# Optimization experiments

Measured on AMD Instinct MI355X. Metric: run time of the kernel, lower is better.

The kernel has to match this reference:

```python
import jax, jax.numpy as jnp
import numpy as np


def setup_inputs() -> dict:
    key = jax.random.key(0)
    k1, k2, k3, k4 = jax.random.split(key, 4)
    B, T, C, H = 32, 2048, 384, 64
    x = jax.random.normal(k1, (B, T, C), dtype=jnp.float32)
    # nn.Linear(C, H, bias=False): weight stored [H, C], applied as x @ W.T.
    # We store the transposed [C, H] form directly.
    s = 1.0 / np.sqrt(C)
    Wk = jax.random.normal(k2, (C, H), dtype=jnp.float32) * s
    Wq = jax.random.normal(k3, (C, H), dtype=jnp.float32) * s
    Wv = jax.random.normal(k4, (C, H), dtype=jnp.float32) * s
    return {"x": x, "Wk": Wk, "Wq": Wq, "Wv": Wv}


def reference(x, Wk, Wq, Wv):
    # x: [B, T, C]; Wk/Wq/Wv: [C, H]
    T = x.shape[1]
    H = Wk.shape[1]
    k = jnp.einsum('btc,ch->bth', x, Wk)
    q = jnp.einsum('btc,ch->bth', x, Wq)
    v = jnp.einsum('btc,ch->bth', x, Wv)
    scale = H ** (-0.5)
    scores = jnp.einsum('bth,bsh->bts', q, k) * scale  # [B, T, T]
    causal = jnp.tril(jnp.ones((T, T), dtype=bool))
    scores = jnp.where(causal, scores, -jnp.inf)
    attn = jax.nn.softmax(scores, axis=-1)
    # dropout is identity in eval mode
    out = jnp.einsum('bts,bsh->bth', attn, v)  # [B, T, H]
    return out
```

## Files before the change

kernel.cpp:

```cpp
#include <hip/hip_runtime.h>

typedef __bf16 bf16_8 __attribute__((ext_vector_type(8)));
typedef __bf16 bf16_4 __attribute__((ext_vector_type(4)));
typedef float  f32x4  __attribute__((ext_vector_type(4)));

#define NB 32
#define NT 2048
#define NC 384
#define NH 64

static __device__ __forceinline__ f32x4 mfma16(bf16_8 a, bf16_8 b, f32x4 c) {
  return __builtin_amdgcn_mfma_f32_16x16x32_bf16(a, b, c, 0, 0, 0);
}

__global__ void pack_w_kernel(const float* __restrict__ Wk, const float* __restrict__ Wq,
                              const float* __restrict__ Wv, __bf16* __restrict__ Wt) {
  int idx = blockIdx.x * 256 + threadIdx.x;
  if (idx >= 192 * NC) return;
  int n = idx / NC, k = idx % NC;
  int sel = n >> 6, h = n & 63;
  const float* W = (sel == 0) ? Wq : (sel == 1 ? Wk : Wv);
  float v = W[k * NH + h];
  if (sel == 0) v *= 0.125f;
  Wt[idx] = (__bf16)v;
}

__launch_bounds__(256)
__global__ void qkv_kernel(const float* __restrict__ x, const __bf16* __restrict__ Wt,
                           __bf16* __restrict__ Q, __bf16* __restrict__ K,
                           __bf16* __restrict__ Vt) {
  __shared__ __bf16 Vl[64][136];

  const int tid  = threadIdx.x;
  const int lane = tid & 63, wq = tid >> 6;
  const int quad = lane >> 4, l16 = lane & 15;
  const int rowblk = blockIdx.x * 128;
  const int rbase  = rowblk + wq * 32;

  f32x4 acc[2][12];
  #pragma unroll
  for (int m = 0; m < 2; ++m)
    #pragma unroll
    for (int n = 0; n < 12; ++n) acc[m][n] = f32x4{0.f, 0.f, 0.f, 0.f};

  for (int kc = 0; kc < 12; ++kc) {
    const int k0 = kc * 32 + quad * 8;
    bf16_8 a[2];
    #pragma unroll
    for (int m = 0; m < 2; ++m) {
      const float* xp = x + (size_t)(rbase + m * 16 + l16) * NC + k0;
      f32x4 x0 = *(const f32x4*)xp;
      f32x4 x1 = *(const f32x4*)(xp + 4);
      bf16_8 t;
      t[0] = (__bf16)x0[0]; t[1] = (__bf16)x0[1]; t[2] = (__bf16)x0[2]; t[3] = (__bf16)x0[3];
      t[4] = (__bf16)x1[0]; t[5] = (__bf16)x1[1]; t[6] = (__bf16)x1[2]; t[7] = (__bf16)x1[3];
      a[m] = t;
    }
    #pragma unroll
    for (int n = 0; n < 12; ++n) {
      bf16_8 b = *(const bf16_8*)(Wt + (size_t)(n * 16 + l16) * NC + k0);
      acc[0][n] = mfma16(a[0], b, acc[0][n]);
      acc[1][n] = mfma16(a[1], b, acc[1][n]);
    }
  }

  #pragma unroll
  for (int m = 0; m < 2; ++m)
    #pragma unroll
    for (int n = 0; n < 8; ++n)
      #pragma unroll
      for (int r = 0; r < 4; ++r) {
        int row = rbase + m * 16 + quad * 4 + r;
        int h = (n & 3) * 16 + l16;
        __bf16 bv = (__bf16)acc[m][n][r];
        if (n < 4) Q[(size_t)row * NH + h] = bv;
        else       K[(size_t)row * NH + h] = bv;
      }

  #pragma unroll
  for (int m = 0; m < 2; ++m)
    #pragma unroll
    for (int n = 8; n < 12; ++n) {
      int h = (n - 8) * 16 + l16;
      int t0 = wq * 32 + m * 16 + quad * 4;
      bf16_4 p;
      p[0] = (__bf16)acc[m][n][0]; p[1] = (__bf16)acc[m][n][1];
      p[2] = (__bf16)acc[m][n][2]; p[3] = (__bf16)acc[m][n][3];
      *(bf16_4*)&Vl[h][t0] = p;
    }
  __syncthreads();
  {
    int h = tid >> 2, seg = tid & 3;
    int bb = rowblk >> 11, t0 = (rowblk & (NT - 1)) + seg * 32;
    const __bf16* src = &Vl[h][seg * 32];
    __bf16* dst = Vt + ((size_t)(bb * NH + h)) * NT + t0;
    #pragma unroll
    for (int i = 0; i < 4; ++i) ((uint4*)dst)[i] = ((const uint4*)src)[i];
  }
}

__launch_bounds__(256)
__global__ void attn_kernel(const __bf16* __restrict__ Q, const __bf16* __restrict__ K,
                            const __bf16* __restrict__ Vt, float* __restrict__ out) {
  __shared__ __bf16 Ks[64][72];
  __shared__ __bf16 Vs[64][72];
  __shared__ __bf16 Ps[4][16][72];

  const int tid  = threadIdx.x;
  const int lane = tid & 63, wq = tid >> 6;
  const int quad = lane >> 4, l16 = lane & 15;
  const int b  = blockIdx.x >> 5;
  const int qt = 31 - (blockIdx.x & 31);
  const int q0 = qt * 64;

  const float NEG_INF = -__builtin_inff();

  const __bf16* qrow = Q + ((size_t)(b * NT + q0 + wq * 16 + l16)) * NH + quad * 8;
  bf16_8 qf0 = *(const bf16_8*)qrow;
  bf16_8 qf1 = *(const bf16_8*)(qrow + 32);

  f32x4 o[4];
  #pragma unroll
  for (int i = 0; i < 4; ++i) o[i] = f32x4{0.f, 0.f, 0.f, 0.f};
  float m_i = NEG_INF, l_i = 0.f;

  const int r = tid >> 2, seg = tid & 3;
  const __bf16* Kg = K  + (size_t)b * NT * NH;
  const __bf16* Vg = Vt + (size_t)b * NH * NT;

  for (int s0 = 0; s0 <= q0; s0 += 64) {
    __syncthreads();
    {
      const uint4* sK = (const uint4*)(Kg + (size_t)(s0 + r) * NH + seg * 16);
      uint4 k0v = sK[0], k1v = sK[1];
      *(uint4*)&Ks[r][seg * 16]     = k0v;
      *(uint4*)&Ks[r][seg * 16 + 8] = k1v;
      const uint4* sV = (const uint4*)(Vg + (size_t)r * NT + s0 + seg * 16);
      uint4 v0v = sV[0], v1v = sV[1];
      *(uint4*)&Vs[r][seg * 16]     = v0v;
      *(uint4*)&Vs[r][seg * 16 + 8] = v1v;
    }
    __syncthreads();

    f32x4 s[4];
    #pragma unroll
    for (int st = 0; st < 4; ++st) {
      bf16_8 a0 = *(const bf16_8*)&Ks[st * 16 + l16][quad * 8];
      bf16_8 a1 = *(const bf16_8*)&Ks[st * 16 + l16][quad * 8 + 32];
      f32x4 accv = f32x4{0.f, 0.f, 0.f, 0.f};
      accv = mfma16(a0, qf0, accv);
      accv = mfma16(a1, qf1, accv);
      s[st] = accv;
    }

    if (s0 == q0) {
      int qg = wq * 16 + l16;
      #pragma unroll
      for (int st = 0; st < 4; ++st)
        #pragma unroll
        for (int rr = 0; rr < 4; ++rr) {
          int sg = st * 16 + quad * 4 + rr;
          if (sg > qg) s[st][rr] = NEG_INF;
        }
    }

    float mx = NEG_INF;
    #pragma unroll
    for (int st = 0; st < 4; ++st)
      #pragma unroll
      for (int rr = 0; rr < 4; ++rr) mx = fmaxf(mx, s[st][rr]);
    mx = fmaxf(mx, __shfl_xor(mx, 16));
    mx = fmaxf(mx, __shfl_xor(mx, 32));
    float m_new = fmaxf(m_i, mx);
    float alpha = __expf(m_i - m_new);

    float lsum = 0.f;
    #pragma unroll
    for (int st = 0; st < 4; ++st) {
      bf16_4 pk;
      #pragma unroll
      for (int rr = 0; rr < 4; ++rr) {
        float p = __expf(s[st][rr] - m_new);
        lsum += p;
        pk[rr] = (__bf16)p;
      }
      *(bf16_4*)&Ps[wq][l16][st * 16 + quad * 4] = pk;
    }
    lsum += __shfl_xor(lsum, 16);
    lsum += __shfl_xor(lsum, 32);
    l_i = l_i * alpha + lsum;
    m_i = m_new;

    f32x4 av;
    #pragma unroll
    for (int rr = 0; rr < 4; ++rr) av[rr] = __shfl(alpha, quad * 4 + rr);
    #pragma unroll
    for (int nt = 0; nt < 4; ++nt)
      #pragma unroll
      for (int rr = 0; rr < 4; ++rr) o[nt][rr] *= av[rr];

    bf16_8 pa0 = *(const bf16_8*)&Ps[wq][l16][quad * 8];
    bf16_8 pa1 = *(const bf16_8*)&Ps[wq][l16][quad * 8 + 32];
    #pragma unroll
    for (int nt = 0; nt < 4; ++nt) {
      bf16_8 b0 = *(const bf16_8*)&Vs[nt * 16 + l16][quad * 8];
      bf16_8 b1 = *(const bf16_8*)&Vs[nt * 16 + l16][quad * 8 + 32];
      o[nt] = mfma16(pa0, b0, o[nt]);
      o[nt] = mfma16(pa1, b1, o[nt]);
    }
  }

  f32x4 lv;
  #pragma unroll
  for (int rr = 0; rr < 4; ++rr) lv[rr] = 1.f / __shfl(l_i, quad * 4 + rr);
  float* op = out + ((size_t)(b * NT + q0 + wq * 16 + quad * 4)) * NH + l16;
  #pragma unroll
  for (int nt = 0; nt < 4; ++nt)
    #pragma unroll
    for (int rr = 0; rr < 4; ++rr)
      op[(size_t)rr * NH + nt * 16] = o[nt][rr] * lv[rr];
}

extern "C" void kernel_launch(void* const* d_in, const int* in_sizes, int n_in,
                              void* d_out, int out_size, void* d_ws, size_t ws_size,
                              hipStream_t stream) {
  const float* x  = (const float*)d_in[0];
  const float* Wk = (const float*)d_in[1];
  const float* Wq = (const float*)d_in[2];
  const float* Wv = (const float*)d_in[3];
  float* out = (float*)d_out;

  char* ws = (char*)d_ws;
  __bf16* Wt  = (__bf16*)ws;
  __bf16* Qb  = (__bf16*)(ws + 256 * 1024);
  __bf16* Kb  = Qb + (size_t)NB * NT * NH;
  __bf16* Vtb = Kb + (size_t)NB * NT * NH;

  pack_w_kernel<<<288, 256, 0, stream>>>(Wk, Wq, Wv, Wt);
  qkv_kernel<<<512, 256, 0, stream>>>(x, Wt, Qb, Kb, Vtb);
  attn_kernel<<<NB * 32, 256, 0, stream>>>(Qb, Kb, Vtb, out);
}
```

Before: 256.8 us.

## Double-buffer K/V tiles, pair causal query tiles per block, shrink QKV tiles

The attention kernel now double-buffers K/V tiles in shared memory. Global loads for the next tile are issued before the current tile's compute and written to the other buffer afterwards, which removes one barrier per iteration. Each block now handles a long and a short causal query tile (qt and 31-qt) to balance work across 512 blocks. The QKV projection uses 64-row blocks with register prefetch of x and a 4-wave occupancy hint, doubling the grid. The cost is more LDS per attention block and fewer attention blocks.

Result: faster. 251.3 us (-2.2%).

```diff
diff --git a/kernel.cpp b/kernel.cpp
--- a/kernel.cpp
+++ b/kernel.cpp
@@ -25,200 +25,219 @@
   Wt[idx] = (__bf16)v;
 }
 
-__launch_bounds__(256)
+__launch_bounds__(256, 4)
 __global__ void qkv_kernel(const float* __restrict__ x, const __bf16* __restrict__ Wt,
                            __bf16* __restrict__ Q, __bf16* __restrict__ K,
                            __bf16* __restrict__ Vt) {
-  __shared__ __bf16 Vl[64][136];
+  __shared__ __bf16 Vl[64][72];
 
   const int tid  = threadIdx.x;
   const int lane = tid & 63, wq = tid >> 6;
   const int quad = lane >> 4, l16 = lane & 15;
-  const int rowblk = blockIdx.x * 128;
-  const int rbase  = rowblk + wq * 32;
-
-  f32x4 acc[2][12];
+  const int rowblk = blockIdx.x * 64;
+  const int rbase  = rowblk + wq * 16;
+
+  f32x4 acc[12];
   #pragma unroll
-  for (int m = 0; m < 2; ++m)
-    #pragma unroll
-    for (int n = 0; n < 12; ++n) acc[m][n] = f32x4{0.f, 0.f, 0.f, 0.f};
+  for (int n = 0; n < 12; ++n) acc[n] = f32x4{0.f, 0.f, 0.f, 0.f};
+
+  const float* xrow = x + (size_t)(rbase + l16) * NC;
+  f32x4 x0 = *(const f32x4*)(xrow + quad * 8);
+  f32x4 x1 = *(const f32x4*)(xrow + quad * 8 + 4);
 
   for (int kc = 0; kc < 12; ++kc) {
-    const int k0 = kc * 32 + quad * 8;
-    bf16_8 a[2];
-    #pragma unroll
-    for (int m = 0; m < 2; ++m) {
-      const float* xp = x + (size_t)(rbase + m * 16 + l16) * NC + k0;
-      f32x4 x0 = *(const f32x4*)xp;
-      f32x4 x1 = *(const f32x4*)(xp + 4);
-      bf16_8 t;
-      t[0] = (__bf16)x0[0]; t[1] = (__bf16)x0[1]; t[2] = (__bf16)x0[2]; t[3] = (__bf16)x0[3];
-      t[4] = (__bf16)x1[0]; t[5] = (__bf16)x1[1]; t[6] = (__bf16)x1[2]; t[7] = (__bf16)x1[3];
-      a[m] = t;
-    }
+    f32x4 nx0, nx1;
+    if (kc < 11) {
+      const float* xp = xrow + (kc + 1) * 32 + quad * 8;
+      nx0 = *(const f32x4*)xp;
+      nx1 = *(const f32x4*)(xp + 4);
+    }
+    bf16_8 a;
+    a[0] = (__bf16)x0[0]; a[1] = (__bf16)x0[1]; a[2] = (__bf16)x0[2]; a[3] = (__bf16)x0[3];
+    a[4] = (__bf16)x1[0]; a[5] = (__bf16)x1[1]; a[6] = (__bf16)x1[2]; a[7] = (__bf16)x1[3];
+    const __bf16* wp = Wt + (size_t)l16 * NC + kc * 32 + quad * 8;
     #pragma unroll
     for (int n = 0; n < 12; ++n) {
-      bf16_8 b = *(const bf16_8*)(Wt + (size_t)(n * 16 + l16) * NC + k0);
-      acc[0][n] = mfma16(a[0], b, acc[0][n]);
-      acc[1][n] = mfma16(a[1], b, acc[1][n]);
-    }
+      bf16_8 b = *(const bf16_8*)(wp + (size_t)n * 16 * NC);
+      acc[n] = mfma16(a, b, acc[n]);
+    }
+    x0 = nx0; x1 = nx1;
   }
 
   #pragma unroll
-  for (int m = 0; m < 2; ++m)
-    #pragma unroll
-    for (int n = 0; n < 8; ++n)
-      #pragma unroll
-      for (int r = 0; r < 4; ++r) {
-        int row = rbase + m * 16 + quad * 4 + r;
-        int h = (n & 3) * 16 + l16;
-        __bf16 bv = (__bf16)acc[m][n][r];
-        if (n < 4) Q[(size_t)row * NH + h] = bv;
-        else       K[(size_t)row * NH + h] = bv;
-      }
+  for (int n = 0; n < 8; ++n)
+    #pragma unroll
+    for (int r = 0; r < 4; ++r) {
+      int row = rbase + quad * 4 + r;
+      int h = (n & 3) * 16 + l16;
+      __bf16 bv = (__bf16)acc[n][r];
+      if (n < 4) Q[(size_t)row * NH + h] = bv;
+      else       K[(size_t)row * NH + h] = bv;
+    }
 
   #pragma unroll
-  for (int m = 0; m < 2; ++m)
-    #pragma unroll
-    for (int n = 8; n < 12; ++n) {
-      int h = (n - 8) * 16 + l16;
-      int t0 = wq * 32 + m * 16 + quad * 4;
-      bf16_4 p;
-      p[0] = (__bf16)acc[m][n][0]; p[1] = (__bf16)acc[m][n][1];
-      p[2] = (__bf16)acc[m][n][2]; p[3] = (__bf16)acc[m][n][3];
-      *(bf16_4*)&Vl[h][t0] = p;
-    }
+  for (int n = 8; n < 12; ++n) {
+    int h = (n - 8) * 16 + l16;
+    int t0 = wq * 16 + quad * 4;
+    bf16_4 p;
+    p[0] = (__bf16)acc[n][0]; p[1] = (__bf16)acc[n][1];
+    p[2] = (__bf16)acc[n][2]; p[3] = (__bf16)acc[n][3];
+    *(bf16_4*)&Vl[h][t0] = p;
+  }
   __syncthreads();
   {
     int h = tid >> 2, seg = tid & 3;
-    int bb = rowblk >> 11, t0 = (rowblk & (NT - 1)) + seg * 32;
-    const __bf16* src = &Vl[h][seg * 32];
+    int bb = rowblk >> 11, t0 = (rowblk & (NT - 1)) + seg * 16;
+    const __bf16* src = &Vl[h][seg * 16];
     __bf16* dst = Vt + ((size_t)(bb * NH + h)) * NT + t0;
-    #pragma unroll
-    for (int i = 0; i < 4; ++i) ((uint4*)dst)[i] = ((const uint4*)src)[i];
+    ((uint4*)dst)[0] = ((const uint4*)src)[0];
+    ((uint4*)dst)[1] = ((const uint4*)src)[1];
   }
 }
 
 __launch_bounds__(256)
 __global__ void attn_kernel(const __bf16* __restrict__ Q, const __bf16* __restrict__ K,
                             const __bf16* __restrict__ Vt, float* __restrict__ out) {
-  __shared__ __bf16 Ks[64][72];
-  __shared__ __bf16 Vs[64][72];
+  __shared__ __bf16 Ks[2][64][72];
+  __shared__ __bf16 Vs[2][64][72];
   __shared__ __bf16 Ps[4][16][72];
 
   const int tid  = threadIdx.x;
   const int lane = tid & 63, wq = tid >> 6;
   const int quad = lane >> 4, l16 = lane & 15;
-  const int b  = blockIdx.x >> 5;
-  const int qt = 31 - (blockIdx.x & 31);
-  const int q0 = qt * 64;
+  const int b    = blockIdx.x >> 4;
+  const int pair = blockIdx.x & 15;
 
   const float NEG_INF = -__builtin_inff();
-
-  const __bf16* qrow = Q + ((size_t)(b * NT + q0 + wq * 16 + l16)) * NH + quad * 8;
-  bf16_8 qf0 = *(const bf16_8*)qrow;
-  bf16_8 qf1 = *(const bf16_8*)(qrow + 32);
-
-  f32x4 o[4];
-  #pragma unroll
-  for (int i = 0; i < 4; ++i) o[i] = f32x4{0.f, 0.f, 0.f, 0.f};
-  float m_i = NEG_INF, l_i = 0.f;
-
   const int r = tid >> 2, seg = tid & 3;
   const __bf16* Kg = K  + (size_t)b * NT * NH;
   const __bf16* Vg = Vt + (size_t)b * NH * NT;
 
-  for (int s0 = 0; s0 <= q0; s0 += 64) {
+  for (int pass = 0; pass < 2; ++pass) {
+    const int qt = pass ? pair : (31 - pair);
+    const int q0 = qt * 64;
+    const int nIter = qt + 1;
+
+    const __bf16* qrow = Q + ((size_t)(b * NT + q0 + wq * 16 + l16)) * NH + quad * 8;
+    bf16_8 qf0 = *(const bf16_8*)qrow;
+    bf16_8 qf1 = *(const bf16_8*)(qrow + 32);
+
+    f32x4 o[4];
+    #pragma unroll
+    for (int i = 0; i < 4; ++i) o[i] = f32x4{0.f, 0.f, 0.f, 0.f};
+    float m_i = NEG_INF, l_i = 0.f;
+
     __syncthreads();
+
     {
-      const uint4* sK = (const uint4*)(Kg + (size_t)(s0 + r) * NH + seg * 16);
-      uint4 k0v = sK[0], k1v = sK[1];
-      *(uint4*)&Ks[r][seg * 16]     = k0v;
-      *(uint4*)&Ks[r][seg * 16 + 8] = k1v;
-      const uint4* sV = (const uint4*)(Vg + (size_t)r * NT + s0 + seg * 16);
-      uint4 v0v = sV[0], v1v = sV[1];
-      *(uint4*)&Vs[r][seg * 16]     = v0v;
-      *(uint4*)&Vs[r][seg * 16 + 8] = v1v;
-    }
-    __syncthreads();
-
-    f32x4 s[4];
-    #pragma unroll
-    for (int st = 0; st < 4; ++st) {
-      bf16_8 a0 = *(const bf16_8*)&Ks[st * 16 + l16][quad * 8];
-      bf16_8 a1 = *(const bf16_8*)&Ks[st * 16 + l16][quad * 8 + 32];
-      f32x4 accv = f32x4{0.f, 0.f, 0.f, 0.f};
-      accv = mfma16(a0, qf0, accv);
-      accv = mfma16(a1, qf1, accv);
-      s[st] = accv;
-    }
-
-    if (s0 == q0) {
-      int qg = wq * 16 + l16;
+      const uint4* sK = (const uint4*)(Kg + (size_t)r * NH + seg * 16);
+      uint4 ka = sK[0], kb = sK[1];
+      const uint4* sV = (const uint4*)(Vg + (size_t)r * NT + seg * 16);
+      uint4 va = sV[0], vb = sV[1];
+      *(uint4*)&Ks[0][r][seg * 16]     = ka;
+      *(uint4*)&Ks[0][r][seg * 16 + 8] = kb;
+      *(uint4*)&Vs[0][r][seg * 16]     = va;
+      *(uint4*)&Vs[0][r][seg * 16 + 8] = vb;
+    }
+
+    for (int i = 0; i < nIter; ++i) {
+      const int cur = i & 1;
+      const bool more = (i + 1 < nIter);
+      uint4 nka, nkb, nva, nvb;
+      if (more) {
+        const int s0n = (i + 1) * 64;
+        const uint4* sK = (const uint4*)(Kg + (size_t)(s0n + r) * NH + seg * 16);
+        nka = sK[0]; nkb = sK[1];
+        const uint4* sV = (const uint4*)(Vg + (size_t)r * NT + s0n + seg * 16);
+        nva = sV[0]; nvb = sV[1];
+      }
+      __syncthreads();
+
+      f32x4 s[4];
+      #pragma unroll
+      for (int st = 0; st < 4; ++st) {
+        bf16_8 a0 = *(const bf16_8*)&Ks[cur][st * 16 + l16][quad * 8];
+        bf16_8 a1 = *(const bf16_8*)&Ks[cur][st * 16 + l16][quad * 8 + 32];
+        f32x4 accv = f32x4{0.f, 0.f, 0.f, 0.f};
+        accv = mfma16(a0, qf0, accv);
+        accv = mfma16(a1, qf1, accv);
+        s[st] = accv;
+      }
+
+      if (i == qt) {
+        int qg = wq * 16 + l16;
+        #pragma unroll
+        for (int st = 0; st < 4; ++st)
+          #pragma unroll
+          for (int rr = 0; rr < 4; ++rr) {
+            int sg = st * 16 + quad * 4 + rr;
+            if (sg > qg) s[st][rr] = NEG_INF;
+          }
+      }
+
+      float mx = NEG_INF;
       #pragma unroll
       for (int st = 0; st < 4; ++st)
         #pragma unroll
+        for (int rr = 0; rr < 4; ++rr) mx = fmaxf(mx, s[st][rr]);
+      mx = fmaxf(mx, __shfl_xor(mx, 16));
+      mx = fmaxf(mx, __shfl_xor(mx, 32));
+      float m_new = fmaxf(m_i, mx);
+      float alpha = __expf(m_i - m_new);
+
+      float lsum = 0.f;
+      #pragma unroll
+      for (int st = 0; st < 4; ++st) {
+        bf16_4 pk;
+        #pragma unroll
         for (int rr = 0; rr < 4; ++rr) {
-          int sg = st * 16 + quad * 4 + rr;
-          if (sg > qg) s[st][rr] = NEG_INF;
+          float p = __expf(s[st][rr] - m_new);
+          lsum += p;
+          pk[rr] = (__bf16)p;
         }
-    }
-
-    float mx = NEG_INF;
-    #pragma unroll
-    for (int st = 0; st < 4; ++st)
-      #pragma unroll
-      for (int rr = 0; rr < 4; ++rr) mx = fmaxf(mx, s[st][rr]);
-    mx = fmaxf(mx, __shfl_xor(mx, 16));
-    mx = fmaxf(mx, __shfl_xor(mx, 32));
-    float m_new = fmaxf(m_i, mx);
-    float alpha = __expf(m_i - m_new);
-
-    float lsum = 0.f;
-    #pragma unroll
-    for (int st = 0; st < 4; ++st) {
-      bf16_4 pk;
-      #pragma unroll
-      for (int rr = 0; rr < 4; ++rr) {
-        float p = __expf(s[st][rr] - m_new);
-        lsum += p;
-        pk[rr] = (__bf16)p;
-      }
-      *(bf16_4*)&Ps[wq][l16][st * 16 + quad * 4] = pk;
-    }
-    lsum += __shfl_xor(lsum, 16);
-    lsum += __shfl_xor(lsum, 32);
-    l_i = l_i * alpha + lsum;
-    m_i = m_new;
-
-    f32x4 av;
-    #pragma unroll
-    for (int rr = 0; rr < 4; ++rr) av[rr] = __shfl(alpha, quad * 4 + rr);
+        *(bf16_4*)&Ps[wq][l16][st * 16 + quad * 4] = pk;
+      }
+      lsum += __shfl_xor(lsum, 16);
+      lsum += __shfl_xor(lsum, 32);
+      l_i = l_i * alpha + lsum;
+      m_i = m_new;
+
+      f32x4 av;
+      #pragma unroll
+      for (int rr = 0; rr < 4; ++rr) av[rr] = __shfl(alpha, quad * 4 + rr);
+      #pragma unroll
+      for (int nt = 0; nt < 4; ++nt)
+        #pragma unroll
+        for (int rr = 0; rr < 4; ++rr) o[nt][rr] *= av[rr];
+
+      bf16_8 pa0 = *(const bf16_8*)&Ps[wq][l16][quad * 8];
+      bf16_8 pa1 = *(const bf16_8*)&Ps[wq][l16][quad * 8 + 32];
+      #pragma unroll
+      for (int nt = 0; nt < 4; ++nt) {
+        bf16_8 b0 = *(const bf16_8*)&Vs[cur][nt * 16 + l16][quad * 8];
+        bf16_8 b1 = *(const bf16_8*)&Vs[cur][nt * 16 + l16][quad * 8 + 32];
+        o[nt] = mfma16(pa0, b0, o[nt]);
+        o[nt] = mfma16(pa1, b1, o[nt]);
+      }
+
+      if (more) {
+        *(uint4*)&Ks[1 - cur][r][seg * 16]     = nka;
+        *(uint4*)&Ks[1 - cur][r][seg * 16 + 8] = nkb;
+        *(uint4*)&Vs[1 - cur][r][seg * 16]     = nva;
+        *(uint4*)&Vs[1 - cur][r][seg * 16 + 8] = nvb;
+      }
+    }
+
+    f32x4 lv;
+    #pragma unroll
+    for (int rr = 0; rr < 4; ++rr) lv[rr] = 1.f / __shfl(l_i, quad * 4 + rr);
+    float* op = out + ((size_t)(b * NT + q0 + wq * 16 + quad * 4)) * NH + l16;
     #pragma unroll
     for (int nt = 0; nt < 4; ++nt)
       #pragma unroll
-      for (int rr = 0; rr < 4; ++rr) o[nt][rr] *= av[rr];
-
-    bf16_8 pa0 = *(const bf16_8*)&Ps[wq][l16][quad * 8];
-    bf16_8 pa1 = *(const bf16_8*)&Ps[wq][l16][quad * 8 + 32];
-    #pragma unroll
-    for (int nt = 0; nt < 4; ++nt) {
-      bf16_8 b0 = *(const bf16_8*)&Vs[nt * 16 + l16][quad * 8];
-      bf16_8 b1 = *(const bf16_8*)&Vs[nt * 16 + l16][quad * 8 + 32];
-      o[nt] = mfma16(pa0, b0, o[nt]);
-      o[nt] = mfma16(pa1, b1, o[nt]);
-    }
-  }
-
-  f32x4 lv;
-  #pragma unroll
-  for (int rr = 0; rr < 4; ++rr) lv[rr] = 1.f / __shfl(l_i, quad * 4 + rr);
-  float* op = out + ((size_t)(b * NT + q0 + wq * 16 + quad * 4)) * NH + l16;
-  #pragma unroll
-  for (int nt = 0; nt < 4; ++nt)
-    #pragma unroll
-    for (int rr = 0; rr < 4; ++rr)
-      op[(size_t)rr * NH + nt * 16] = o[nt][rr] * lv[rr];
+      for (int rr = 0; rr < 4; ++rr)
+        op[(size_t)rr * NH + nt * 16] = o[nt][rr] * lv[rr];
+  }
 }
 
 extern "C" void kernel_launch(void* const* d_in, const int* in_sizes, int n_in,
@@ -237,6 +256,6 @@
   __bf16* Vtb = Kb + (size_t)NB * NT * NH;
 
   pack_w_kernel<<<288, 256, 0, stream>>>(Wk, Wq, Wv, Wt);
-  qkv_kernel<<<512, 256, 0, stream>>>(x, Wt, Qb, Kb, Vtb);
-  attn_kernel<<<NB * 32, 256, 0, stream>>>(Qb, Kb, Vtb, out);
-}
+  qkv_kernel<<<1024, 256, 0, stream>>>(x, Wt, Qb, Kb, Vtb);
+  attn_kernel<<<NB * 16, 256, 0, stream>>>(Qb, Kb, Vtb, out);
+}
```
